# Kernel optimization log

Hardware: AMD Instinct MI355X
Metric: run time of the kernel (lower is better)

The kernel has to match this reference:

```python
import jax, jax.numpy as jnp
import numpy as np
from jax import lax

B = 4096
D = 128
N = 81
H = 4
HD = D // H


def _conv(x, w, b, pad):
    y = lax.conv_general_dilated(x, w, (1, 1), [(pad, pad), (pad, pad)],
                                 dimension_numbers=('NCHW', 'OIHW', 'NCHW'))
    return y + b[None, :, None, None]


def _attn_mask():
    # per-head additive structural mask: same-row, same-col, same-box, global
    idx = jnp.arange(N)
    rows, cols = idx // 9, idx % 9
    boxes = rows // 3 * 3 + cols // 3
    same = lambda v: (v[:, None] == v[None, :]).astype(jnp.float32)
    return jnp.stack([same(rows), same(cols), same(boxes),
                      jnp.ones((N, N), jnp.float32)], 0)  # [4, 81, 81]


def setup_inputs():
    key = jax.random.key(0)
    ks = jax.random.split(key, 12)
    digits = jax.random.randint(ks[0], (B, 9, 9), 0, 10)
    s = jax.nn.one_hot(digits, 10, axis=1, dtype=jnp.float32)  # [B,10,9,9]

    def w(k, shape, fan):
        return jax.random.normal(k, shape, jnp.float32) / np.sqrt(fan)

    return {
        's': s,
        'c1_w': w(ks[1], (64, 10, 1, 1), 10), 'c1_b': jnp.zeros((64,)),
        'c2_w': w(ks[2], (128, 64, 3, 3), 64 * 9), 'c2_b': jnp.zeros((128,)),
        'c3_w': w(ks[3], (128, 128, 3, 3), 128 * 9), 'c3_b': jnp.zeros((128,)),
        'emb': 0.02 * jax.random.normal(ks[4], (1, N, D), jnp.float32),
        'in_w': w(ks[5], (3 * D, D), D), 'in_b': jnp.zeros((3 * D,)),
        'out_w': w(ks[6], (D, D), D), 'out_b': jnp.zeros((D,)),
        'ln_g': jnp.ones((D,)), 'ln_b': jnp.zeros((D,)),
        'l1_w': w(ks[7], (D, D), D), 'l1_b': jnp.zeros((D,)),
        'l2_w': w(ks[8], (D, D), D), 'l2_b': jnp.zeros((D,)),
        'pos_w': w(ks[9], (1, D), D), 'pos_b': jnp.zeros((1,)),
        'num_w': w(ks[10], (10, D), D), 'num_b': jnp.zeros((10,)),
    }


def reference(s, c1_w, c1_b, c2_w, c2_b, c3_w, c3_b, emb, in_w, in_b,
              out_w, out_b, ln_g, ln_b, l1_w, l1_b, l2_w, l2_b,
              pos_w, pos_b, num_w, num_b):
    # conv stem (note: no activation after c1, matching the torch code)
    x = _conv(s, c1_w, c1_b, 0)
    x = jax.nn.silu(_conv(x, c2_w, c2_b, 1))
    x = jax.nn.silu(_conv(x, c3_w, c3_b, 1))
    x = x.reshape(B, D, N).transpose(0, 2, 1) + emb  # [B,81,128]

    # MHA with per-head additive structural mask, no residual
    qkv = x @ in_w.T + in_b
    q, k, v = jnp.split(qkv, 3, axis=-1)
    heads = lambda t: t.reshape(B, N, H, HD).transpose(0, 2, 1, 3)
    q, k, v = heads(q), heads(k), heads(v)
    scores = jnp.einsum('bhqd,bhkd->bhqk', q, k) / np.sqrt(HD) + _attn_mask()[None]
    a = jax.nn.softmax(scores, axis=-1)          # [B,4,81,81]
    asc = a.mean(axis=1)                          # averaged attn weights
    ctx = jnp.einsum('bhqk,bhkd->bhqd', a, v).transpose(0, 2, 1, 3).reshape(B, N, D)
    x = ctx @ out_w.T + out_b

    # LayerNorm
    mu = x.mean(-1, keepdims=True)
    var = ((x - mu) ** 2).mean(-1, keepdims=True)
    x = (x - mu) / jnp.sqrt(var + 1e-5) * ln_g + ln_b

    x = jax.nn.silu(x @ l1_w.T + l1_b)
    x = jax.nn.silu(x @ l2_w.T + l2_b)

    # position head with masked softmax over empty cells
    pos_logits = (x @ pos_w.T + pos_b)[..., 0]    # [B,81]
    given = (s.argmax(1) != 0).reshape(B, N)
    pos_logits = jnp.where(given, -1e9, pos_logits)
    k1, k2 = jax.random.split(jax.random.key(42))
    pos = jax.random.categorical(k1, pos_logits)  # [B] int

    # number head at sampled position, digit 0 masked out
    num_logits = x @ num_w.T + num_b              # [B,81,10]
    o = jnp.take_along_axis(num_logits, pos[:, None, None], axis=1)[:, 0, :]
    o = o.at[:, 0].set(-jnp.inf)
    num = jax.random.categorical(k2, o)
    return pos, num, asc
```

## Files before the change

kernel.cpp:

```cpp
#include <hip/hip_runtime.h>
#include <stdint.h>
#include <math.h>


#define NB 4096

typedef unsigned short u16;
typedef _Float16 f16x8 __attribute__((ext_vector_type(8)));
typedef float f32x4 __attribute__((ext_vector_type(4)));

__device__ __forceinline__ float silu_f(float v) {
  return v / (1.0f + expf(-v));
}

__device__ __forceinline__ void splitu(float v, u16& h, u16& l) {
  _Float16 hf = (_Float16)v;
  _Float16 lf = (_Float16)((v - (float)hf) * 2048.0f);
  union { _Float16 f; u16 u; } a, b;
  a.f = hf; b.f = lf;
  h = a.u; l = b.u;
}

__device__ __forceinline__ float joinu(u16 h, u16 l) {
  union { u16 u; _Float16 f; } a, b;
  a.u = h; b.u = l;
  return (float)a.f + (float)b.f * (1.f/2048.f);
}

__device__ __forceinline__ void tf_round(uint32_t& x0, uint32_t& x1, int r) {
  x0 += x1;
  x1 = (x1 << r) | (x1 >> (32 - r));
  x1 ^= x0;
}

__device__ __forceinline__ void threefry2x32(uint32_t k0, uint32_t k1,
                                             uint32_t x0, uint32_t x1,
                                             uint32_t& o0, uint32_t& o1) {
  uint32_t k2 = k0 ^ k1 ^ 0x1BD11BDAu;
  x0 += k0; x1 += k1;
  tf_round(x0,x1,13); tf_round(x0,x1,15); tf_round(x0,x1,26); tf_round(x0,x1,6);
  x0 += k1; x1 += k2 + 1u;
  tf_round(x0,x1,17); tf_round(x0,x1,29); tf_round(x0,x1,16); tf_round(x0,x1,24);
  x0 += k2; x1 += k0 + 2u;
  tf_round(x0,x1,13); tf_round(x0,x1,15); tf_round(x0,x1,26); tf_round(x0,x1,6);
  x0 += k0; x1 += k1 + 3u;
  tf_round(x0,x1,17); tf_round(x0,x1,29); tf_round(x0,x1,16); tf_round(x0,x1,24);
  x0 += k1; x1 += k2 + 4u;
  tf_round(x0,x1,13); tf_round(x0,x1,15); tf_round(x0,x1,26); tf_round(x0,x1,6);
  x0 += k2; x1 += k0 + 5u;
  o0 = x0; o1 = x1;
}

__device__ __forceinline__ void jax_split42(uint32_t& k1a, uint32_t& k1b,
                                            uint32_t& k2a, uint32_t& k2b) {
  threefry2x32(0u, 42u, 0u, 0u, k1a, k1b);
  threefry2x32(0u, 42u, 0u, 1u, k2a, k2b);
}

__device__ __forceinline__ uint32_t jax_randbits(uint32_t ka, uint32_t kb,
                                                 uint32_t i) {
  uint32_t o0, o1;
  threefry2x32(ka, kb, 0u, i, o0, o1);
  return o0 ^ o1;
}

__device__ __forceinline__ float jax_gumbel_bits(uint32_t bits) {
  float f = __uint_as_float((bits >> 9) | 0x3f800000u) - 1.0f;
  const float tiny = 1.17549435e-38f;
  float u = fmaxf(tiny, f + tiny);
  return -logf(-logf(u));
}

__global__ __launch_bounds__(256) void k_prep(
    const float* __restrict__ c1_w, const float* __restrict__ c1_b,
    const float* __restrict__ c2_w, const float* __restrict__ c3_w,
    const float* __restrict__ in_w,
    const float* __restrict__ out_w, const float* __restrict__ l1_w,
    const float* __restrict__ l2_w,
    float* __restrict__ T2e, u16* __restrict__ WAh, u16* __restrict__ WAl,
    u16* __restrict__ WIh, u16* __restrict__ WIl,
    u16* __restrict__ WOh, u16* __restrict__ W1h, u16* __restrict__ W2h)
{
  int idx = blockIdx.x * 256 + threadIdx.x;
  if (idx < 9*11*128) {
    int oc = idx & 127;
    int t  = idx >> 7;
    int g  = t % 11;
    int d  = t / 11;
    float acc = 0.f;
    if (g < 10) {
      int di = d / 3, dj = d % 3;
      for (int ic = 0; ic < 64; ++ic) {
        float x1 = c1_w[ic*10 + g] + c1_b[ic];
        acc += c2_w[((oc*64 + ic)*3 + di)*3 + dj] * x1;
      }
    }
    T2e[idx] = acc;
  } else if (idx < 160128) {
    int j  = idx - 12672;
    int jj = j & 7;
    int t  = j >> 3;
    int ln = t & 63;
    int t2 = t >> 6;
    int ot = t2 & 7;
    int t3 = t2 >> 3;
    int kc = t3 & 3;
    int d  = t3 >> 2;
    int oc = ot*16 + (ln & 15);
    int ic = kc*32 + (ln >> 4)*8 + jj;
    float w = c3_w[(oc*128 + ic)*9 + d];
    u16 wh, wl;
    splitu(w, wh, wl);
    WAh[j] = wh; WAl[j] = wl;
  } else if (idx < 209280) {
    int j = idx - 160128;
    int mi = j >> 14;
    int jr = j & 16383;
    int jj = jr & 7;
    int t  = jr >> 3;
    int ln = t & 63;
    int t2 = t >> 6;
    int ot = t2 & 7;
    int kc = t2 >> 3;
    int oc = ot*16 + (ln & 15);
    int k  = kc*32 + (ln >> 4)*8 + jj;
    const float* W = (mi == 0) ? out_w : (mi == 1) ? l1_w : l2_w;
    u16* Dh = (mi == 0) ? WOh : (mi == 1) ? W1h : W2h;
    u16 wh, wl;
    splitu(W[oc*128 + k], wh, wl);
    Dh[jr] = wh; Dh[16384 + jr] = wl;
  } else if (idx < 258432) {
    int j  = idx - 209280;
    int jj = j & 7;
    int t  = j >> 3;
    int ln = t & 63;
    int t2 = t >> 6;
    int kc = t2 & 3;
    int t3 = t2 >> 2;
    int h  = t3 / 6;
    int pu = t3 - h*6;
    int part = pu >> 1, sub = pu & 1;
    int row = part*128 + h*32 + sub*16 + (ln & 15);
    int k   = kc*32 + (ln >> 4)*8 + jj;
    u16 wh, wl;
    splitu(in_w[row*128 + k], wh, wl);
    WIh[j] = wh; WIl[j] = wl;
  }
}

__global__ __launch_bounds__(256, 2) void k_stem(
    const float* __restrict__ s, const float* __restrict__ T2e,
    const float* __restrict__ c2_b,
    const u16* __restrict__ WAh, const u16* __restrict__ WAl,
    const float* __restrict__ c3_b, const float* __restrict__ emb,
    u16* __restrict__ xh, u16* __restrict__ xl, int* __restrict__ digits)
{
  __shared__ __align__(16) u16 x2h[121*128];
  __shared__ __align__(16) u16 x2l[121*128];
  __shared__ int dg[121];
  const int b   = blockIdx.x;
  const int tid = threadIdx.x;

  for (int i = tid; i < 1936; i += 256) {
    ((uint4*)x2h)[i] = make_uint4(0u,0u,0u,0u);
    ((uint4*)x2l)[i] = make_uint4(0u,0u,0u,0u);
  }
  if (tid < 121) dg[tid] = 10;
  __syncthreads();

  if (tid < 81) {
    const float* sp = s + (size_t)b*810 + tid;
    float dv = 0.f;
    #pragma unroll
    for (int c = 1; c < 10; ++c) dv += (float)c * sp[c*81];
    int d = (int)(dv + 0.5f);
    dg[(tid/9 + 1)*11 + (tid%9 + 1)] = d;
    digits[b*81 + tid] = d;
  }
  __syncthreads();

  for (int i = tid; i < 1296; i += 256) {
    const int p  = i >> 4;
    const int k8 = i & 15;
    const int r0 = p / 9, c0 = p - r0*9;
    const float4 b0 = *(const float4*)(c2_b + k8*8);
    const float4 b1 = *(const float4*)(c2_b + k8*8 + 4);
    float a0=b0.x, a1=b0.y, a2=b0.z, a3=b0.w;
    float a4=b1.x, a5=b1.y, a6=b1.z, a7=b1.w;
    #pragma unroll
    for (int d = 0; d < 9; ++d) {
      const int g = dg[(r0 + d/3)*11 + (c0 + d%3)];
      const float* tp = T2e + (size_t)(d*11 + g)*128 + k8*8;
      const float4 t0 = *(const float4*)tp;
      const float4 t1 = *(const float4*)(tp + 4);
      a0 += t0.x; a1 += t0.y; a2 += t0.z; a3 += t0.w;
      a4 += t1.x; a5 += t1.y; a6 += t1.z; a7 += t1.w;
    }
    float v[8];
    v[0]=silu_f(a0); v[1]=silu_f(a1); v[2]=silu_f(a2); v[3]=silu_f(a3);
    v[4]=silu_f(a4); v[5]=silu_f(a5); v[6]=silu_f(a6); v[7]=silu_f(a7);
    f16x8 hv, lv;
    #pragma unroll
    for (int j = 0; j < 8; ++j) {
      _Float16 h = (_Float16)v[j];
      hv[j] = h;
      lv[j] = (_Float16)((v[j] - (float)h) * 2048.0f);
    }
    const int row = (r0 + 1)*11 + (c0 + 1);
    const uint32_t bo = (uint32_t)row*256u + ((uint32_t)(k8 ^ (row & 15)) << 4);
    *(f16x8*)((char*)x2h + bo) = hv;
    *(f16x8*)((char*)x2l + bo) = lv;
  }
  __syncthreads();

  const int ln  = tid & 63;
  const int wv  = tid >> 6;
  const int lg  = ln >> 4;
  const int lr  = ln & 15;
  const int otB = (wv & 1) * 4;
  const int ntB = (wv >> 1) * 3;

  f32x4 accH[4][3];
  f32x4 accC[4][3];
  #pragma unroll
  for (int ot = 0; ot < 4; ++ot)
    #pragma unroll
    for (int nt = 0; nt < 3; ++nt) {
      accH[ot][nt] = (f32x4){0.f,0.f,0.f,0.f};
      accC[ot][nt] = (f32x4){0.f,0.f,0.f,0.f};
    }

  int pbase[3];
  #pragma unroll
  for (int nt = 0; nt < 3; ++nt) {
    const int c = (ntB + nt)*16 + lr;
    pbase[nt] = (c < 81) ? (c/9)*11 + (c%9) : 0;
  }
  const char* x2hB = (const char*)x2h;
  const char* x2lB = (const char*)x2l;

  for (int d = 0; d < 9; ++d) {
    const int off = (d/3)*11 + (d - (d/3)*3);
    int rowv[3];
    #pragma unroll
    for (int nt = 0; nt < 3; ++nt) rowv[nt] = pbase[nt] + off;
    #pragma unroll
    for (int kc = 0; kc < 4; ++kc) {
      f16x8 Bh[3], Bl[3];
      #pragma unroll
      for (int nt = 0; nt < 3; ++nt) {
        const uint32_t o = (uint32_t)rowv[nt]*256u +
            ((uint32_t)((kc*4 + lg) ^ (rowv[nt] & 15)) << 4);
        Bh[nt] = *(const f16x8*)(x2hB + o);
        Bl[nt] = *(const f16x8*)(x2lB + o);
      }
      const int abase = (((d*4 + kc)*8 + otB)*64 + ln)*8;
      f16x8 Ah[4], Al[4];
      #pragma unroll
      for (int ot = 0; ot < 4; ++ot) {
        Ah[ot] = *(const f16x8*)(WAh + abase + ot*512);
        Al[ot] = *(const f16x8*)(WAl + abase + ot*512);
      }
      #pragma unroll
      for (int ot = 0; ot < 4; ++ot)
        #pragma unroll
        for (int nt = 0; nt < 3; ++nt) {
          accH[ot][nt] = __builtin_amdgcn_mfma_f32_16x16x32_f16(
              Ah[ot], Bh[nt], accH[ot][nt], 0, 0, 0);
          accC[ot][nt] = __builtin_amdgcn_mfma_f32_16x16x32_f16(
              Ah[ot], Bl[nt], accC[ot][nt], 0, 0, 0);
          accC[ot][nt] = __builtin_amdgcn_mfma_f32_16x16x32_f16(
              Al[ot], Bh[nt], accC[ot][nt], 0, 0, 0);
        }
    }
  }

  #pragma unroll
  for (int nt = 0; nt < 3; ++nt) {
    const int cell = (ntB + nt)*16 + lr;
    if (cell < 81) {
      const size_t xoff = ((size_t)b*81 + cell)*128;
      #pragma unroll
      for (int ot = 0; ot < 4; ++ot) {
        const int oc = (otB + ot)*16 + lg*4;
        const float4 b3 = *(const float4*)(c3_b + oc);
        const float4 e  = *(const float4*)(emb + cell*128 + oc);
        const f32x4 hh = accH[ot][nt];
        const f32x4 cc = accC[ot][nt];
        float o0 = silu_f(hh[0] + cc[0]*(1.f/2048.f) + b3.x) + e.x;
        float o1 = silu_f(hh[1] + cc[1]*(1.f/2048.f) + b3.y) + e.y;
        float o2 = silu_f(hh[2] + cc[2]*(1.f/2048.f) + b3.z) + e.z;
        float o3 = silu_f(hh[3] + cc[3]*(1.f/2048.f) + b3.w) + e.w;
        ushort4 hv, lv;
        splitu(o0, hv.x, lv.x); splitu(o1, hv.y, lv.y);
        splitu(o2, hv.z, lv.z); splitu(o3, hv.w, lv.w);
        *(ushort4*)(xh + xoff + oc) = hv;
        *(ushort4*)(xl + xoff + oc) = lv;
      }
    }
  }
}

#define ATTN_LDS_BYTES 141568

__global__ __launch_bounds__(512, 1) void k_attn(
    const u16* __restrict__ xhg, const u16* __restrict__ xlg,
    const u16* __restrict__ WIh, const u16* __restrict__ WIl,
    const float* __restrict__ in_b,
    u16* __restrict__ ctxh, u16* __restrict__ ctxl, float* __restrict__ asc)
{
  extern __shared__ char smc[];
  char*  XH   = smc;
  char*  XL   = smc + 24576;
  char*  QK   = smc + 49152;
  char*  VTH  = smc + 73728;
  char*  VTL  = smc + 81920;
  float* SC   = (float*)(smc + 90112);
  char*  PH   = smc + 90112;
  char*  PL   = smc + 114688;
  uint32_t* RCB = (uint32_t*)(smc + 141184);

  const int b   = blockIdx.x;
  const int tid = threadIdx.x;
  const int ln  = tid & 63;
  const int wv  = tid >> 6;
  const int lg  = ln >> 4;
  const int lr  = ln & 15;

  if (tid < 96) {
    const int r = tid/9, c = tid - r*9;
    const int bx = (r/3)*3 + c/3;
    RCB[tid] = (uint32_t)r | ((uint32_t)c << 8) | ((uint32_t)bx << 16);
  }
  {
    const u16* gx = xhg + (size_t)b*81*128;
    const u16* gl = xlg + (size_t)b*81*128;
    for (int i = tid; i < 1296; i += 512) {
      const int n = i >> 4, k8 = i & 15;
      const uint4 hv = *(const uint4*)(gx + n*128 + k8*8);
      const uint4 lv = *(const uint4*)(gl + n*128 + k8*8);
      const uint32_t bo = (uint32_t)n*256u + ((uint32_t)(k8 ^ (n & 15)) << 4);
      *(uint4*)(XH + bo) = hv;
      *(uint4*)(XL + bo) = lv;
    }
    for (int i = tid; i < 480; i += 512) {
      char* base = (i < 240) ? XH : XL;
      const int j = (i < 240) ? i : (i - 240);
      *(uint4*)(base + 81*256 + j*16) = make_uint4(0u,0u,0u,0u);
    }
  }

  const int srow = tid >> 2;
  const int ssub = tid & 3;
  const int skn  = (ssub == 3) ? 9 : 24;
  float ascR[24];
  #pragma unroll
  for (int i = 0; i < 24; ++i) ascR[i] = 0.f;

  __syncthreads();

  for (int h = 0; h < 4; ++h) {
    {
      const int t0 = (wv*36) >> 3, t1 = ((wv + 1)*36) >> 3;
      int curNt = -1;
      f16x8 Bh[4], Bl[4];
      for (int u = t0; u < t1; ++u) {
        const int nt = u/6, pu = u - (u/6)*6;
        if (nt != curNt) {
          curNt = nt;
          const int row = nt*16 + lr;
          #pragma unroll
          for (int kc = 0; kc < 4; ++kc) {
            const uint32_t o = (uint32_t)row*256u +
                ((uint32_t)((kc*4 + lg) ^ (row & 15)) << 4);
            Bh[kc] = *(const f16x8*)(XH + o);
            Bl[kc] = *(const f16x8*)(XL + o);
          }
        }
        const int part = pu >> 1, sub = pu & 1;
        const int rowbase = part*128 + h*32 + sub*16;
        const u16* wph = WIh + (size_t)((h*6 + pu)*4)*512 + ln*8;
        const u16* wpl = WIl + (size_t)((h*6 + pu)*4)*512 + ln*8;
        f32x4 aH = (f32x4){0.f,0.f,0.f,0.f};
        f32x4 aC = (f32x4){0.f,0.f,0.f,0.f};
        #pragma unroll
        for (int kc = 0; kc < 4; ++kc) {
          const f16x8 Ah = *(const f16x8*)(wph + kc*512);
          const f16x8 Al = *(const f16x8*)(wpl + kc*512);
          aH = __builtin_amdgcn_mfma_f32_16x16x32_f16(Ah, Bh[kc], aH, 0,0,0);
          aC = __builtin_amdgcn_mfma_f32_16x16x32_f16(Ah, Bl[kc], aC, 0,0,0);
          aC = __builtin_amdgcn_mfma_f32_16x16x32_f16(Al, Bh[kc], aC, 0,0,0);
        }
        const float4 bia = *(const float4*)(in_b + rowbase + lg*4);
        const float v0 = aH[0] + aC[0]*(1.f/2048.f) + bia.x;
        const float v1 = aH[1] + aC[1]*(1.f/2048.f) + bia.y;
        const float v2 = aH[2] + aC[2]*(1.f/2048.f) + bia.z;
        const float v3 = aH[3] + aC[3]*(1.f/2048.f) + bia.w;
        const int cell = nt*16 + lr;
        if (part < 2) {
          ushort4 hw, lw;
          splitu(v0, hw.x, lw.x); splitu(v1, hw.y, lw.y);
          splitu(v2, hw.z, lw.z); splitu(v3, hw.w, lw.w);
          const int sflat = part*4 + sub*2 + (lg >> 1);
          const int byo   = (lg & 1)*8;
          const uint32_t adH = (uint32_t)cell*256u +
              ((uint32_t)(sflat ^ (cell & 15)) << 4) + byo;
          const uint32_t adL = (uint32_t)cell*256u +
              ((uint32_t)((8 + sflat) ^ (cell & 15)) << 4) + byo;
          *(ushort4*)(QK + adH) = hw;
          *(ushort4*)(QK + adL) = lw;
        } else {
          const float vv[4] = {v0, v1, v2, v3};
          #pragma unroll
          for (int r = 0; r < 4; ++r) {
            const int hd = sub*16 + lg*4 + r;
            u16 hh, llv;
            splitu(vv[r], hh, llv);
            const uint32_t ad = (uint32_t)hd*256u +
                ((uint32_t)((cell >> 3) ^ (hd & 15)) << 4) + (cell & 7)*2;
            *(u16*)(VTH + ad) = hh;
            *(u16*)(VTL + ad) = llv;
          }
        }
      }
    }
    __syncthreads();

    {
      const uint32_t mb = (h==0) ? 0xFFu : (h==1) ? 0xFF00u
                        : (h==2) ? 0xFF0000u : 0u;
      const int t0 = (wv*36) >> 3, t1 = ((wv + 1)*36) >> 3;
      for (int t = t0; t < t1; ++t) {
        const int qt = t/6, nt = t - (t/6)*6;
        const int ra = qt*16 + lr;
        const f16x8 Qh = *(const f16x8*)(QK + (uint32_t)ra*256u +
            ((uint32_t)(lg ^ (ra & 15)) << 4));
        const f16x8 Ql = *(const f16x8*)(QK + (uint32_t)ra*256u +
            ((uint32_t)((8 + lg) ^ (ra & 15)) << 4));
        const int rb = nt*16 + lr;
        const f16x8 Kh = *(const f16x8*)(QK + (uint32_t)rb*256u +
            ((uint32_t)((4 + lg) ^ (rb & 15)) << 4));
        const f16x8 Kl = *(const f16x8*)(QK + (uint32_t)rb*256u +
            ((uint32_t)((12 + lg) ^ (rb & 15)) << 4));
        f32x4 aH = (f32x4){0.f,0.f,0.f,0.f};
        f32x4 aC = (f32x4){0.f,0.f,0.f,0.f};
        aH = __builtin_amdgcn_mfma_f32_16x16x32_f16(Qh, Kh, aH, 0,0,0);
        aC = __builtin_amdgcn_mfma_f32_16x16x32_f16(Qh, Kl, aC, 0,0,0);
        aC = __builtin_amdgcn_mfma_f32_16x16x32_f16(Ql, Kh, aC, 0,0,0);
        const int kcell = nt*16 + lr;
        const uint32_t kk = RCB[kcell];
        #pragma unroll
        for (int r = 0; r < 4; ++r) {
          const int q = qt*16 + lg*4 + r;
          const uint32_t qq = RCB[q];
          const float msk = (((qq ^ kk) & mb) == 0u) ? 1.f : 0.f;
          SC[q*132 + kcell] =
              (aH[r] + aC[r]*(1.f/2048.f)) * 0.17677669529663687f + msk;
        }
      }
    }
    __syncthreads();

    float e[24];
    float rinv = 0.f;
    if (tid < 324) {
      const float* sr = SC + srow*132 + ssub*24;
      #pragma unroll
      for (int q4 = 0; q4 < 6; ++q4) {
        const float4 v = *(const float4*)(sr + q4*4);
        e[q4*4+0] = v.x; e[q4*4+1] = v.y; e[q4*4+2] = v.z; e[q4*4+3] = v.w;
      }
      float m = -1e30f;
      #pragma unroll
      for (int c = 0; c < 24; ++c)
        if (c < skn) m = fmaxf(m, e[c]);
      m = fmaxf(m, __shfl_xor(m, 1));
      m = fmaxf(m, __shfl_xor(m, 2));
      float ss = 0.f;
      #pragma unroll
      for (int c = 0; c < 24; ++c) {
        const float ex = (c < skn) ? __expf(e[c] - m) : 0.f;
        e[c] = ex;
        ss += ex;
      }
      ss += __shfl_xor(ss, 1);
      ss += __shfl_xor(ss, 2);
      rinv = 1.0f / ss;
    }
    __syncthreads();
    if (tid < 324) {
      #pragma unroll
      for (int cc = 0; cc < 3; ++cc) {
        const int c8 = ssub*3 + cc;
        union { u16 u[8]; uint4 v; } hw, lw;
        #pragma unroll
        for (int j = 0; j < 8; ++j) {
          const float p = e[cc*8 + j] * rinv;
          ascR[cc*8 + j] += p;
          splitu(p, hw.u[j], lw.u[j]);
        }
        const uint32_t ad = (uint32_t)srow*256u +
            ((uint32_t)(c8 ^ (srow & 15)) << 4);
        *(uint4*)(PH + ad) = hw.v;
        *(uint4*)(PL + ad) = lw.v;
      }
    }
    __syncthreads();

    for (int t = wv; t < 12; t += 8) {
      const int ot = t/6, nt = t - (t/6)*6;
      f32x4 aH = (f32x4){0.f,0.f,0.f,0.f};
      f32x4 aC = (f32x4){0.f,0.f,0.f,0.f};
      #pragma unroll
      for (int kc = 0; kc < 3; ++kc) {
        const int ra = ot*16 + lr;
        const uint32_t oa = (uint32_t)ra*256u +
            ((uint32_t)((kc*4 + lg) ^ (ra & 15)) << 4);
        const f16x8 Vh = *(const f16x8*)(VTH + oa);
        const f16x8 Vl = *(const f16x8*)(VTL + oa);
        const int rb = nt*16 + lr;
        const uint32_t ob = (uint32_t)rb*256u +
            ((uint32_t)((kc*4 + lg) ^ (rb & 15)) << 4);
        const f16x8 Pf  = *(const f16x8*)(PH + ob);
        const f16x8 Pl2 = *(const f16x8*)(PL + ob);
        aH = __builtin_amdgcn_mfma_f32_16x16x32_f16(Vh, Pf,  aH, 0,0,0);
        aC = __builtin_amdgcn_mfma_f32_16x16x32_f16(Vh, Pl2, aC, 0,0,0);
        aC = __builtin_amdgcn_mfma_f32_16x16x32_f16(Vl, Pf,  aC, 0,0,0);
      }
      const int cell = nt*16 + lr;
      if (cell < 81) {
        const size_t co = ((size_t)b*81 + cell)*128 + h*32 + ot*16 + lg*4;
        ushort4 hw, lw;
        float r0 = aH[0] + aC[0]*(1.f/2048.f);
        float r1 = aH[1] + aC[1]*(1.f/2048.f);
        float r2 = aH[2] + aC[2]*(1.f/2048.f);
        float r3 = aH[3] + aC[3]*(1.f/2048.f);
        splitu(r0, hw.x, lw.x); splitu(r1, hw.y, lw.y);
        splitu(r2, hw.z, lw.z); splitu(r3, hw.w, lw.w);
        *(ushort4*)(ctxh + co) = hw;
        *(ushort4*)(ctxl + co) = lw;
      }
    }
    __syncthreads();
  }

  if (tid < 324) {
    float* ap = asc + (size_t)b*6561 + srow*81 + ssub*24;
    #pragma unroll
    for (int c = 0; c < 24; ++c)
      if (c < skn) ap[c] = 0.25f * ascR[c];
  }
}

#define POST_LDS_BYTES 105664

__global__ __launch_bounds__(512, 1) void k_post(
    const u16* __restrict__ ctxh, const u16* __restrict__ ctxl,
    const u16* __restrict__ WOh,  const float* __restrict__ out_b,
    const float* __restrict__ ln_g, const float* __restrict__ ln_b,
    const u16* __restrict__ W1h,  const float* __restrict__ l1_b,
    const u16* __restrict__ W2h,  const float* __restrict__ l2_b,
    const float* __restrict__ pos_w, const float* __restrict__ pos_b,
    const float* __restrict__ num_w, const float* __restrict__ num_b,
    const int* __restrict__ digits,  float* __restrict__ dout)
{
  extern __shared__ char smc[];
  char*  YH   = smc;
  char*  YL   = smc + 24576;
  char*  ZH   = smc + 49152;
  char*  ZL   = smc + 73728;
  float* red1 = (float*)(smc + 98304);
  float* red2 = (float*)(smc + 101376);
  float* mu   = (float*)(smc + 104448);
  float* rstd = (float*)(smc + 104832);
  float* vals = (float*)(smc + 105216);
  int*   posi = (int*)(smc + 105600);

  const int b   = blockIdx.x;
  const int tid = threadIdx.x;
  const int ln  = tid & 63;
  const int wv  = tid >> 6;
  const int lg  = ln >> 4;
  const int lr  = ln & 15;
  const int ocb = wv*16 + lg*4;

  {
    const u16* gh = ctxh + (size_t)b*81*128;
    const u16* gl = ctxl + (size_t)b*81*128;
    for (int i = tid; i < 1296; i += 512) {
      const int n = i >> 4, k8 = i & 15;
      const uint4 hv = *(const uint4*)(gh + n*128 + k8*8);
      const uint4 lv = *(const uint4*)(gl + n*128 + k8*8);
      const uint32_t bo = (uint32_t)n*256u + ((uint32_t)(k8 ^ (n & 15)) << 4);
      *(uint4*)(YH + bo) = hv;
      *(uint4*)(YL + bo) = lv;
    }
    for (int i = tid; i < 480; i += 512) {
      char* base = (i < 240) ? YH : YL;
      const int j = (i < 240) ? i : (i - 240);
      *(uint4*)(base + 81*256 + j*16) = make_uint4(0u,0u,0u,0u);
    }
  }
  __syncthreads();

  f32x4 aH[6], aC[6];
  #define GEMM6(BH, BL, WT)                                               \
    {                                                                     \
      _Pragma("unroll")                                                   \
      for (int nt = 0; nt < 6; ++nt) {                                    \
        aH[nt] = (f32x4){0.f,0.f,0.f,0.f};                                \
        aC[nt] = (f32x4){0.f,0.f,0.f,0.f};                                \
      }                                                                   \
      for (int kc = 0; kc < 4; ++kc) {                                    \
        const int ab = ((kc*8 + wv)*64 + ln)*8;                           \
        const f16x8 Ah = *(const f16x8*)((WT) + ab);                      \
        const f16x8 Al = *(const f16x8*)((WT) + 16384 + ab);              \
        _Pragma("unroll")                                                 \
        for (int nt = 0; nt < 6; ++nt) {                                  \
          const int row = nt*16 + lr;                                     \
          const uint32_t o = (uint32_t)row*256u +                         \
              ((uint32_t)((kc*4 + lg) ^ (row & 15)) << 4);                \
          const f16x8 Bh = *(const f16x8*)((BH) + o);                     \
          const f16x8 Bl = *(const f16x8*)((BL) + o);                     \
          aH[nt] = __builtin_amdgcn_mfma_f32_16x16x32_f16(Ah, Bh, aH[nt], 0,0,0); \
          aC[nt] = __builtin_amdgcn_mfma_f32_16x16x32_f16(Ah, Bl, aC[nt], 0,0,0); \
          aC[nt] = __builtin_amdgcn_mfma_f32_16x16x32_f16(Al, Bh, aC[nt], 0,0,0); \
        }                                                                 \
      }                                                                   \
    }

  GEMM6(YH, YL, WOh);
  float y[6][4];
  {
    const float4 bv = *(const float4*)(out_b + ocb);
    #pragma unroll
    for (int nt = 0; nt < 6; ++nt) {
      y[nt][0] = aH[nt][0] + aC[nt][0]*(1.f/2048.f) + bv.x;
      y[nt][1] = aH[nt][1] + aC[nt][1]*(1.f/2048.f) + bv.y;
      y[nt][2] = aH[nt][2] + aC[nt][2]*(1.f/2048.f) + bv.z;
      y[nt][3] = aH[nt][3] + aC[nt][3]*(1.f/2048.f) + bv.w;
    }
  }

  #pragma unroll
  for (int nt = 0; nt < 6; ++nt) {
    float s1 = y[nt][0] + y[nt][1] + y[nt][2] + y[nt][3];
    s1 += __shfl_xor(s1, 16);
    s1 += __shfl_xor(s1, 32);
    if (ln < 16) red1[(nt*16 + lr)*8 + wv] = s1;
  }
  __syncthreads();
  if (tid < 96) {
    float s = 0.f;
    #pragma unroll
    for (int w = 0; w < 8; ++w) s += red1[tid*8 + w];
    mu[tid] = s * (1.0f/128.0f);
  }
  __syncthreads();
  #pragma unroll
  for (int nt = 0; nt < 6; ++nt) {
    const float m = mu[nt*16 + lr];
    float d0 = y[nt][0]-m, d1 = y[nt][1]-m, d2 = y[nt][2]-m, d3 = y[nt][3]-m;
    float s2 = d0*d0 + d1*d1 + d2*d2 + d3*d3;
    s2 += __shfl_xor(s2, 16);
    s2 += __shfl_xor(s2, 32);
    if (ln < 16) red2[(nt*16 + lr)*8 + wv] = s2;
  }
  __syncthreads();
  if (tid < 96) {
    float s = 0.f;
    #pragma unroll
    for (int w = 0; w < 8; ++w) s += red2[tid*8 + w];
    rstd[tid] = 1.0f / sqrtf(s * (1.0f/128.0f) + 1e-5f);
  }
  __syncthreads();
  {
    const float4 g  = *(const float4*)(ln_g + ocb);
    const float4 bb = *(const float4*)(ln_b + ocb);
    #pragma unroll
    for (int nt = 0; nt < 6; ++nt) {
      const int cell = nt*16 + lr;
      const float m = mu[cell], rs = rstd[cell];
      float z0 = (y[nt][0]-m)*rs*g.x + bb.x;
      float z1 = (y[nt][1]-m)*rs*g.y + bb.y;
      float z2 = (y[nt][2]-m)*rs*g.z + bb.z;
      float z3 = (y[nt][3]-m)*rs*g.w + bb.w;
      ushort4 hw, lw;
      splitu(z0, hw.x, lw.x); splitu(z1, hw.y, lw.y);
      splitu(z2, hw.z, lw.z); splitu(z3, hw.w, lw.w);
      const uint32_t ad = (uint32_t)cell*256u +
          ((uint32_t)((wv*2 + (lg >> 1)) ^ (cell & 15)) << 4) + (lg & 1)*8;
      *(ushort4*)(ZH + ad) = hw;
      *(ushort4*)(ZL + ad) = lw;
    }
  }
  __syncthreads();

  GEMM6(ZH, ZL, W1h);
  {
    const float4 bv = *(const float4*)(l1_b + ocb);
    #pragma unroll
    for (int nt = 0; nt < 6; ++nt) {
      const int cell = nt*16 + lr;
      float z0 = silu_f(aH[nt][0] + aC[nt][0]*(1.f/2048.f) + bv.x);
      float z1 = silu_f(aH[nt][1] + aC[nt][1]*(1.f/2048.f) + bv.y);
      float z2 = silu_f(aH[nt][2] + aC[nt][2]*(1.f/2048.f) + bv.z);
      float z3 = silu_f(aH[nt][3] + aC[nt][3]*(1.f/2048.f) + bv.w);
      ushort4 hw, lw;
      splitu(z0, hw.x, lw.x); splitu(z1, hw.y, lw.y);
      splitu(z2, hw.z, lw.z); splitu(z3, hw.w, lw.w);
      const uint32_t ad = (uint32_t)cell*256u +
          ((uint32_t)((wv*2 + (lg >> 1)) ^ (cell & 15)) << 4) + (lg & 1)*8;
      *(ushort4*)(YH + ad) = hw;
      *(ushort4*)(YL + ad) = lw;
    }
  }
  __syncthreads();

  GEMM6(YH, YL, W2h);
  {
    const float4 bv = *(const float4*)(l2_b + ocb);
    const float4 pw = *(const float4*)(pos_w + ocb);
    #pragma unroll
    for (int nt = 0; nt < 6; ++nt) {
      const int cell = nt*16 + lr;
      float z0 = silu_f(aH[nt][0] + aC[nt][0]*(1.f/2048.f) + bv.x);
      float z1 = silu_f(aH[nt][1] + aC[nt][1]*(1.f/2048.f) + bv.y);
      float z2 = silu_f(aH[nt][2] + aC[nt][2]*(1.f/2048.f) + bv.z);
      float z3 = silu_f(aH[nt][3] + aC[nt][3]*(1.f/2048.f) + bv.w);
      ushort4 hw, lw;
      splitu(z0, hw.x, lw.x); splitu(z1, hw.y, lw.y);
      splitu(z2, hw.z, lw.z); splitu(z3, hw.w, lw.w);
      const uint32_t ad = (uint32_t)cell*256u +
          ((uint32_t)((wv*2 + (lg >> 1)) ^ (cell & 15)) << 4) + (lg & 1)*8;
      *(ushort4*)(ZH + ad) = hw;
      *(ushort4*)(ZL + ad) = lw;
      float ps = z0*pw.x + z1*pw.y + z2*pw.z + z3*pw.w;
      ps += __shfl_xor(ps, 16);
      ps += __shfl_xor(ps, 32);
      if (ln < 16) red1[cell*8 + wv] = ps;
    }
  }
  __syncthreads();

  uint32_t k1a, k1b, k2a, k2b;
  jax_split42(k1a, k1b, k2a, k2b);

  if (tid < 81) {
    float acc = pos_b[0];
    #pragma unroll
    for (int w = 0; w < 8; ++w) acc += red1[tid*8 + w];
    if (digits[b*81 + tid] != 0) acc = -1e9f;
    uint32_t bits = jax_randbits(k1a, k1b, (uint32_t)(b*81 + tid));
    vals[tid] = acc + jax_gumbel_bits(bits);
  }
  __syncthreads();
  if (tid == 0) {
    float best = vals[0]; int bi = 0;
    for (int n = 1; n < 81; ++n)
      if (vals[n] > best) { best = vals[n]; bi = n; }
    *posi = bi;
    dout[b] = (float)bi;
  }
  __syncthreads();
  const int pos = *posi;

  if (tid < 80) {
    const int d = tid >> 3, j = tid & 7;
    float ssum = 0.f;
    #pragma unroll
    for (int c = 0; c < 16; ++c) {
      const int k = j*16 + c;
      const uint32_t ad = (uint32_t)pos*256u +
          ((uint32_t)((k >> 3) ^ (pos & 15)) << 4) + (k & 7)*2;
      const float yv = joinu(*(const u16*)(ZH + ad), *(const u16*)(ZL + ad));
      ssum += yv * num_w[d*128 + k];
    }
    red2[tid] = ssum;
  }
  __syncthreads();
  if (tid < 10) {
    float acc = num_b[tid];
    #pragma unroll
    for (int j = 0; j < 8; ++j) acc += red2[tid*8 + j];
    if (tid == 0) acc = -INFINITY;
    uint32_t bits = jax_randbits(k2a, k2b, (uint32_t)(b*10 + tid));
    vals[tid] = acc + jax_gumbel_bits(bits);
  }
  __syncthreads();
  if (tid == 0) {
    float best = vals[0]; int bi = 0;
    for (int d = 1; d < 10; ++d)
      if (vals[d] > best) { best = vals[d]; bi = d; }
    dout[NB + b] = (float)bi;
  }
}

extern "C" void kernel_launch(void* const* d_in, const int* in_sizes, int n_in,
                              void* d_out, int out_size, void* d_ws, size_t ws_size,
                              hipStream_t stream) {
  const float* s     = (const float*)d_in[0];
  const float* c1_w  = (const float*)d_in[1];
  const float* c1_b  = (const float*)d_in[2];
  const float* c2_w  = (const float*)d_in[3];
  const float* c2_b  = (const float*)d_in[4];
  const float* c3_w  = (const float*)d_in[5];
  const float* c3_b  = (const float*)d_in[6];
  const float* emb   = (const float*)d_in[7];
  const float* in_w  = (const float*)d_in[8];
  const float* in_b  = (const float*)d_in[9];
  const float* out_w = (const float*)d_in[10];
  const float* out_b = (const float*)d_in[11];
  const float* ln_g  = (const float*)d_in[12];
  const float* ln_b  = (const float*)d_in[13];
  const float* l1_w  = (const float*)d_in[14];
  const float* l1_b  = (const float*)d_in[15];
  const float* l2_w  = (const float*)d_in[16];
  const float* l2_b  = (const float*)d_in[17];
  const float* pos_w = (const float*)d_in[18];
  const float* pos_b = (const float*)d_in[19];
  const float* num_w = (const float*)d_in[20];
  const float* num_b = (const float*)d_in[21];

  float* ws     = (float*)d_ws;
  float* T2e    = ws;
  u16*   WAh    = (u16*)(ws + 12672);
  u16*   WAl    = (u16*)(ws + 86400);
  u16*   WOh    = (u16*)(ws + 160128);
  u16*   W1h    = (u16*)(ws + 176512);
  u16*   W2h    = (u16*)(ws + 192896);
  u16*   WIh    = (u16*)(ws + 209280);
  u16*   WIl    = (u16*)(ws + 233856);
  int*   digits = (int*)(ws + 258432);
  u16*   xh     = (u16*)(ws + 541056);
  u16*   xl     = (u16*)(ws + 21774720);
  u16*   ctxh   = (u16*)(ws + 43008384);
  u16*   ctxl   = (u16*)(ws + 43008384 + 21233664);

  float* dout = (float*)d_out;
  float* asc  = dout + 2*NB;

  hipFuncSetAttribute((const void*)k_attn,
                      hipFuncAttributeMaxDynamicSharedMemorySize,
                      ATTN_LDS_BYTES);
  hipFuncSetAttribute((const void*)k_post,
                      hipFuncAttributeMaxDynamicSharedMemorySize,
                      POST_LDS_BYTES);

  k_prep<<<dim3(1010), dim3(256), 0, stream>>>(
      c1_w, c1_b, c2_w, c3_w, in_w, out_w, l1_w, l2_w,
      T2e, WAh, WAl, WIh, WIl, WOh, W1h, W2h);
  k_stem<<<dim3(NB), dim3(256), 0, stream>>>(
      s, T2e, c2_b, WAh, WAl, c3_b, emb, xh, xl, digits);
  k_attn<<<dim3(NB), dim3(512), ATTN_LDS_BYTES, stream>>>(
      xh, xl, WIh, WIl, in_b, ctxh, ctxl, asc);
  k_post<<<dim3(NB), dim3(512), POST_LDS_BYTES, stream>>>(
      ctxh, ctxl, WOh, out_b, ln_g, ln_b, W1h, l1_b, W2h, l2_b,
      pos_w, pos_b, num_w, num_b, digits, dout);
}
```

Measured before the change: 1.421 ms.

## Shrink attention LDS footprint to allow two blocks per CU

Stops staging the x hi/lo tiles in LDS and instead loads the B operands for the QKV projection straight from global memory, with zero-fill for padding rows. The score buffer pitch drops from 132 to 84 floats and the P buffers from 256 to 192-byte rows with a narrower XOR swizzle, bringing LDS use from about 141 KB to about 78 KB. The launch-bounds minimum-blocks hint is removed so more than one block can be resident per CU. In exchange, x is now read from global memory once per task tile rather than once per block, and the narrower swizzle may cause more LDS bank conflicts.

```diff
diff --git a/kernel.cpp b/kernel.cpp
--- a/kernel.cpp
+++ b/kernel.cpp
@@ -301,24 +301,22 @@
   }
 }
 
-#define ATTN_LDS_BYTES 141568
-
-__global__ __launch_bounds__(512, 1) void k_attn(
+#define ATTN_LDS_BYTES 78208
+
+__global__ __launch_bounds__(512) void k_attn(
     const u16* __restrict__ xhg, const u16* __restrict__ xlg,
     const u16* __restrict__ WIh, const u16* __restrict__ WIl,
     const float* __restrict__ in_b,
     u16* __restrict__ ctxh, u16* __restrict__ ctxl, float* __restrict__ asc)
 {
   extern __shared__ char smc[];
-  char*  XH   = smc;
-  char*  XL   = smc + 24576;
-  char*  QK   = smc + 49152;
-  char*  VTH  = smc + 73728;
-  char*  VTL  = smc + 81920;
-  float* SC   = (float*)(smc + 90112);
-  char*  PH   = smc + 90112;
-  char*  PL   = smc + 114688;
-  uint32_t* RCB = (uint32_t*)(smc + 141184);
+  char*  QK   = smc;
+  char*  VTH  = smc + 24576;
+  char*  VTL  = smc + 32768;
+  char*  PH   = smc + 40960;
+  char*  PL   = smc + 59392;
+  float* SC   = (float*)(smc + 40960);
+  uint32_t* RCB = (uint32_t*)(smc + 77824);
 
   const int b   = blockIdx.x;
   const int tid = threadIdx.x;
@@ -331,23 +329,6 @@
     const int r = tid/9, c = tid - r*9;
     const int bx = (r/3)*3 + c/3;
     RCB[tid] = (uint32_t)r | ((uint32_t)c << 8) | ((uint32_t)bx << 16);
-  }
-  {
-    const u16* gx = xhg + (size_t)b*81*128;
-    const u16* gl = xlg + (size_t)b*81*128;
-    for (int i = tid; i < 1296; i += 512) {
-      const int n = i >> 4, k8 = i & 15;
-      const uint4 hv = *(const uint4*)(gx + n*128 + k8*8);
-      const uint4 lv = *(const uint4*)(gl + n*128 + k8*8);
-      const uint32_t bo = (uint32_t)n*256u + ((uint32_t)(k8 ^ (n & 15)) << 4);
-      *(uint4*)(XH + bo) = hv;
-      *(uint4*)(XL + bo) = lv;
-    }
-    for (int i = tid; i < 480; i += 512) {
-      char* base = (i < 240) ? XH : XL;
-      const int j = (i < 240) ? i : (i - 240);
-      *(uint4*)(base + 81*256 + j*16) = make_uint4(0u,0u,0u,0u);
-    }
   }
 
   const int srow = tid >> 2;
@@ -368,13 +349,23 @@
         const int nt = u/6, pu = u - (u/6)*6;
         if (nt != curNt) {
           curNt = nt;
-          const int row = nt*16 + lr;
-          #pragma unroll
-          for (int kc = 0; kc < 4; ++kc) {
-            const uint32_t o = (uint32_t)row*256u +
-                ((uint32_t)((kc*4 + lg) ^ (row & 15)) << 4);
-            Bh[kc] = *(const f16x8*)(XH + o);
-            Bl[kc] = *(const f16x8*)(XL + o);
+          const int cell0 = nt*16 + lr;
+          if (cell0 < 81) {
+            const u16* gx = xhg + ((size_t)b*81 + cell0)*128 + lg*8;
+            const u16* gl = xlg + ((size_t)b*81 + cell0)*128 + lg*8;
+            #pragma unroll
+            for (int kc = 0; kc < 4; ++kc) {
+              Bh[kc] = *(const f16x8*)(gx + kc*32);
+              Bl[kc] = *(const f16x8*)(gl + kc*32);
+            }
+          } else {
+            #pragma unroll
+            for (int kc = 0; kc < 4; ++kc)
+              #pragma unroll
+              for (int j = 0; j < 8; ++j) {
+                Bh[kc][j] = (_Float16)0.f;
+                Bl[kc][j] = (_Float16)0.f;
+              }
           }
         }
         const int part = pu >> 1, sub = pu & 1;
@@ -448,14 +439,16 @@
         aC = __builtin_amdgcn_mfma_f32_16x16x32_f16(Qh, Kl, aC, 0,0,0);
         aC = __builtin_amdgcn_mfma_f32_16x16x32_f16(Ql, Kh, aC, 0,0,0);
         const int kcell = nt*16 + lr;
-        const uint32_t kk = RCB[kcell];
-        #pragma unroll
-        for (int r = 0; r < 4; ++r) {
-          const int q = qt*16 + lg*4 + r;
-          const uint32_t qq = RCB[q];
-          const float msk = (((qq ^ kk) & mb) == 0u) ? 1.f : 0.f;
-          SC[q*132 + kcell] =
-              (aH[r] + aC[r]*(1.f/2048.f)) * 0.17677669529663687f + msk;
+        if (kcell < 81) {
+          const uint32_t kk = RCB[kcell];
+          #pragma unroll
+          for (int r = 0; r < 4; ++r) {
+            const int q = qt*16 + lg*4 + r;
+            const uint32_t qq = RCB[q];
+            const float msk = (((qq ^ kk) & mb) == 0u) ? 1.f : 0.f;
+            SC[q*84 + kcell] =
+                (aH[r] + aC[r]*(1.f/2048.f)) * 0.17677669529663687f + msk;
+          }
         }
       }
     }
@@ -464,7 +457,7 @@
     float e[24];
     float rinv = 0.f;
     if (tid < 324) {
-      const float* sr = SC + srow*132 + ssub*24;
+      const float* sr = SC + srow*84 + ssub*24;
       #pragma unroll
       for (int q4 = 0; q4 < 6; ++q4) {
         const float4 v = *(const float4*)(sr + q4*4);
@@ -499,8 +492,8 @@
           ascR[cc*8 + j] += p;
           splitu(p, hw.u[j], lw.u[j]);
         }
-        const uint32_t ad = (uint32_t)srow*256u +
-            ((uint32_t)(c8 ^ (srow & 15)) << 4);
+        const uint32_t ad = (uint32_t)srow*192u +
+            ((uint32_t)(c8 ^ (srow & 3)) << 4);
         *(uint4*)(PH + ad) = hw.v;
         *(uint4*)(PL + ad) = lw.v;
       }
@@ -519,8 +512,8 @@
         const f16x8 Vh = *(const f16x8*)(VTH + oa);
         const f16x8 Vl = *(const f16x8*)(VTL + oa);
         const int rb = nt*16 + lr;
-        const uint32_t ob = (uint32_t)rb*256u +
-            ((uint32_t)((kc*4 + lg) ^ (rb & 15)) << 4);
+        const uint32_t ob = (uint32_t)rb*192u +
+            ((uint32_t)((kc*4 + lg) ^ (rb & 3)) << 4);
         const f16x8 Pf  = *(const f16x8*)(PH + ob);
         const f16x8 Pl2 = *(const f16x8*)(PL + ob);
         aH = __builtin_amdgcn_mfma_f32_16x16x32_f16(Vh, Pf,  aH, 0,0,0);
```

After: 1.489 ms. 4.8% more time.
